# Kernel tuning notes

Measured on AMD Instinct MI355X. Metric: run time of the kernel, lower is better.

## Reference

```python
import jax, jax.numpy as jnp
import numpy as np


def _l2norm(t, axis=-1, eps=1e-12):
    # matches torch F.normalize: x / max(||x||, eps)
    n = jnp.sqrt(jnp.sum(t * t, axis=axis, keepdims=True))
    return t / jnp.maximum(n, eps)


def setup_inputs() -> dict:
    key = jax.random.key(0)
    ks = jax.random.split(key, 5)
    B, N, C, H = 16, 4096, 768, 12
    x = jax.random.normal(ks[0], (B, N, C), dtype=jnp.float32)
    Wqkv = jax.random.normal(ks[1], (C, 3 * C), dtype=jnp.float32) * (C ** -0.5)
    bqkv = jax.random.normal(ks[2], (3 * C,), dtype=jnp.float32) * 0.02
    Wproj = jax.random.normal(ks[3], (C, C), dtype=jnp.float32) * (C ** -0.5)
    bproj = jax.random.normal(ks[4], (C,), dtype=jnp.float32) * 0.02
    temperature = jnp.ones((H, 1, 1), dtype=jnp.float32)
    return {"x": x, "Wqkv": Wqkv, "bqkv": bqkv, "Wproj": Wproj,
            "bproj": bproj, "temperature": temperature}


def reference(x, Wqkv, bqkv, Wproj, bproj, temperature):
    B, N, C = x.shape
    H = temperature.shape[0]
    Dh = C // H
    qkv = x @ Wqkv + bqkv                      # [B,N,3C]
    qkv = qkv.reshape(B, N, 3, H, Dh)
    # -> [3,B,H,Dh,N] (channels-as-tokens layout)
    qkv = jnp.transpose(qkv, (2, 0, 3, 4, 1))
    q, k, v = qkv[0], qkv[1], qkv[2]           # each [B,H,Dh,N]
    q = _l2norm(q, axis=-1)
    k = _l2norm(k, axis=-1)
    # cross-covariance over channels: [B,H,Dh,Dh]
    attn = jnp.einsum('bhdn,bhen->bhde', q, k) * temperature
    attn = jax.nn.softmax(attn, axis=-1)
    out = jnp.einsum('bhde,bhen->bhdn', attn, v)  # [B,H,Dh,N]
    out = jnp.transpose(out, (0, 3, 1, 2)).reshape(B, N, C)
    return out @ Wproj + bproj
```

## Files before the change

kernel.cpp:

```cpp
#include <hip/hip_runtime.h>

typedef __bf16 bf16x8 __attribute__((ext_vector_type(8)));
typedef float  f32x4  __attribute__((ext_vector_type(4)));
typedef unsigned short u16x8 __attribute__((ext_vector_type(8)));
typedef unsigned short u16x4 __attribute__((ext_vector_type(4)));

#define MFMA16(a, b, c) __builtin_amdgcn_mfma_f32_16x16x32_bf16((a), (b), (c), 0, 0, 0)

#define GLOAD16(g, l) __builtin_amdgcn_global_load_lds( \
    (const __attribute__((address_space(1))) void*)(g),  \
    (__attribute__((address_space(3))) void*)(l), 16, 0, 0)

__device__ __forceinline__ float bf2f(unsigned short u) {
    unsigned int x = ((unsigned int)u) << 16;
    return __builtin_bit_cast(float, x);
}
__device__ __forceinline__ unsigned short f2bf(float f) {
    unsigned int x = __builtin_bit_cast(unsigned int, f);
    x = x + 0x7FFFu + ((x >> 16) & 1u);
    return (unsigned short)(x >> 16);
}
__device__ __forceinline__ bool is_f32(const unsigned short* tf) { return tf[0] == 0; }
__device__ __forceinline__ float ldscal(const void* p, int i, bool f32m) {
    return f32m ? ((const float*)p)[i] : bf2f(((const unsigned short*)p)[i]);
}

__device__ __forceinline__ void tr_tile(const void* in_, unsigned short* out,
                                        int R, int C, int istride,
                                        int bid, bool f32m, unsigned short* T)
{
    const int nct = C >> 6;
    const int tx = bid % nct;
    const int ty = bid / nct;
    const int r0 = ty * 64, c0 = tx * 64;
    const int t = threadIdx.x;
#pragma unroll
    for (int s = 0; s < 2; ++s) {
        const int idx = t + s * 256;
        const int rr = idx >> 3;
        const int cc = (idx & 7) * 8;
        unsigned short v[8];
        if (f32m) {
            const float* inf = (const float*)in_;
            f32x4 a = *(const f32x4*)&inf[(size_t)(r0 + rr) * istride + c0 + cc];
            f32x4 b = *(const f32x4*)&inf[(size_t)(r0 + rr) * istride + c0 + cc + 4];
#pragma unroll
            for (int j = 0; j < 4; ++j) { v[j] = f2bf(a[j]); v[4 + j] = f2bf(b[j]); }
        } else {
            u16x8 a = *(const u16x8*)&((const unsigned short*)in_)[(size_t)(r0 + rr) * istride + c0 + cc];
#pragma unroll
            for (int j = 0; j < 8; ++j) v[j] = a[j];
        }
#pragma unroll
        for (int j = 0; j < 8; ++j) T[(cc + j) * 72 + rr] = v[j];
    }
    __syncthreads();
#pragma unroll
    for (int s = 0; s < 2; ++s) {
        const int idx = t + s * 256;
        const int cc = idx >> 3;
        const int rr = (idx & 7) * 8;
        u16x8 v = *(const u16x8*)&T[cc * 72 + rr];
        *(u16x8*)&out[(size_t)(c0 + cc) * R + r0 + rr] = v;
    }
}

__global__ __launch_bounds__(256)
void prep_all(const void* __restrict__ x, unsigned short* __restrict__ xb,
              unsigned short* __restrict__ xbT, float* __restrict__ sB,
              const void* __restrict__ Wqkv, const void* __restrict__ Wp,
              unsigned short* __restrict__ WqkT, unsigned short* __restrict__ Wv_bf,
              unsigned short* __restrict__ WprojT, const unsigned short* __restrict__ tf)
{
    __shared__ unsigned short T[64 * 72];
    const bool f32m = is_f32(tf);
    if (blockIdx.x < 12288) {
        const int tx = blockIdx.x % 12;
        const int ty = blockIdx.x / 12;
        const int r0 = ty * 64, c0 = tx * 64;
        const int t = threadIdx.x;
#pragma unroll
        for (int s = 0; s < 2; ++s) {
            const int idx = t + s * 256;
            const int rr = idx >> 3;
            const int cc = (idx & 7) * 8;
            u16x8 v;
            if (f32m) {
                const float* inf = (const float*)x;
                f32x4 a = *(const f32x4*)&inf[(size_t)(r0 + rr) * 768 + c0 + cc];
                f32x4 b = *(const f32x4*)&inf[(size_t)(r0 + rr) * 768 + c0 + cc + 4];
#pragma unroll
                for (int j = 0; j < 4; ++j) { v[j] = f2bf(a[j]); v[4 + j] = f2bf(b[j]); }
            } else {
                v = *(const u16x8*)&((const unsigned short*)x)[(size_t)(r0 + rr) * 768 + c0 + cc];
            }
            *(u16x8*)&xb[(size_t)(r0 + rr) * 768 + c0 + cc] = v;
#pragma unroll
            for (int j = 0; j < 8; ++j) T[(cc + j) * 72 + rr] = v[j];
        }
        __syncthreads();
#pragma unroll
        for (int s = 0; s < 2; ++s) {
            const int idx = t + s * 256;
            const int cc = idx >> 3;
            const int rr = (idx & 7) * 8;
            u16x8 v = *(const u16x8*)&T[cc * 72 + rr];
            *(u16x8*)&xbT[(size_t)(c0 + cc) * 65536 + r0 + rr] = v;
        }
        {
            const int col = t >> 2;
            const int seg = t & 3;
            float s = 0.f;
#pragma unroll
            for (int r = 0; r < 16; ++r) s += bf2f(T[col * 72 + seg * 16 + r]);
            s += __shfl_xor(s, 1);
            s += __shfl_xor(s, 2);
            if (seg == 0) atomicAdd(&sB[(r0 >> 12) * 768 + c0 + col], s);
        }
    } else {
        const int bid = blockIdx.x - 12288;
        if (bid < 288) {
            tr_tile(Wqkv, WqkT, 768, 1536, 2304, bid, f32m, T);
        } else if (bid < 576) {
            const int t = (bid - 288) * 256 + threadIdx.x;
            const int c = t / 96;
            const int e0 = (t % 96) * 8;
            u16x8 v;
            if (f32m) {
                const float* p = (const float*)Wqkv + (size_t)c * 2304 + 1536 + e0;
                f32x4 a = *(const f32x4*)p;
                f32x4 b = *(const f32x4*)(p + 4);
#pragma unroll
                for (int j = 0; j < 4; ++j) { v[j] = f2bf(a[j]); v[4 + j] = f2bf(b[j]); }
            } else {
                v = *(const u16x8*)&((const unsigned short*)Wqkv)[(size_t)c * 2304 + 1536 + e0];
            }
            *(u16x8*)&Wv_bf[(size_t)c * 768 + e0] = v;
        } else {
            tr_tile(Wp, WprojT, 768, 768, 768, bid - 576, f32m, T);
        }
    }
}

__global__ __launch_bounds__(256, 2)
void gemmG(const unsigned short* __restrict__ A, unsigned short* __restrict__ G)
{
    constexpr int NT = 64;
    constexpr size_t LD = 65536;
    __shared__ __align__(16) char SM[65536];
    unsigned short* lds = (unsigned short*)SM;

    const int tid  = threadIdx.x;
    const int wave = tid >> 6;
    const int lane = tid & 63;
    const int wm   = wave >> 1;
    const int wn   = wave & 1;
    const int lr   = lane & 15;
    const int lq   = lane >> 4;

    const int per = gridDim.x >> 3;
    const int wg  = (blockIdx.x & 7) * per + (blockIdx.x >> 3);
    const int b = wg / 21;
    int rr21 = wg % 21;
    int mt = 0;
    while (rr21 >= 6 - mt) { rr21 -= 6 - mt; ++mt; }
    const int nt = mt + rr21;
    const size_t m0 = (size_t)mt * 128;
    const int n0 = nt * 128;

    const unsigned short* Ab = A + m0 * LD + (size_t)b * 4096;
    const unsigned short* Bb = A + (size_t)n0 * LD + (size_t)b * 4096;
    unsigned short* Gb = G + (size_t)b * 589824;

    f32x4 zero = {0.f, 0.f, 0.f, 0.f};
    f32x4 acc[4][4];
#pragma unroll
    for (int i = 0; i < 4; ++i)
#pragma unroll
        for (int j = 0; j < 4; ++j) acc[i][j] = zero;

    auto STAGE = [&](int t) {
        unsigned short* la_ = lds + (t & 1) * 16384;
        unsigned short* lb_ = la_ + 8192;
#pragma unroll
        for (int it = 0; it < 4; ++it) {
            const int c = it * 256 + tid;
            const int row = c >> 3;
            const int gs = (c & 7) ^ (row & 7);
            GLOAD16(Ab + (size_t)row * LD + t * 64 + gs * 8, la_ + c * 8);
        }
#pragma unroll
        for (int it = 0; it < 4; ++it) {
            const int c = it * 256 + tid;
            const int row = c >> 3;
            const int gs = (c & 7) ^ (row & 7);
            GLOAD16(Bb + (size_t)row * LD + t * 64 + gs * 8, lb_ + c * 8);
        }
    };

    STAGE(0);
    STAGE(1);

    for (int t = 0; t < NT; ++t) {
        if (t + 1 < NT) asm volatile("s_waitcnt vmcnt(8)" ::: "memory");
        else            asm volatile("s_waitcnt vmcnt(0)" ::: "memory");
        __builtin_amdgcn_s_barrier();
        __builtin_amdgcn_sched_barrier(0);

        const char* la = (const char*)(lds + (t & 1) * 16384);
        const char* lb = la + 16384;

        bf16x8 bfr[4][2], af[4][2];
#pragma unroll
        for (int ni = 0; ni < 4; ++ni)
#pragma unroll
            for (int ks = 0; ks < 2; ++ks) {
                const int row = wn * 64 + ni * 16 + lr;
                const int s   = ks * 4 + lq;
                bfr[ni][ks] = *(const bf16x8*)(lb + row * 128 + ((s ^ (row & 7)) << 4));
            }
#pragma unroll
        for (int mi = 0; mi < 4; ++mi)
#pragma unroll
            for (int ks = 0; ks < 2; ++ks) {
                const int row = wm * 64 + mi * 16 + lr;
                const int s   = ks * 4 + lq;
                af[mi][ks] = *(const bf16x8*)(la + row * 128 + ((s ^ (row & 7)) << 4));
            }
        __builtin_amdgcn_s_setprio(1);
#pragma unroll
        for (int mi = 0; mi < 4; ++mi)
#pragma unroll
            for (int ni = 0; ni < 4; ++ni)
#pragma unroll
                for (int ks = 0; ks < 2; ++ks)
                    acc[mi][ni] = MFMA16(af[mi][ks], bfr[ni][ks], acc[mi][ni]);
        __builtin_amdgcn_s_setprio(0);

        __builtin_amdgcn_sched_barrier(0);
        __builtin_amdgcn_s_barrier();
        if (t + 2 < NT) STAGE(t + 2);
    }

#pragma unroll
    for (int mi = 0; mi < 4; ++mi)
#pragma unroll
        for (int ni = 0; ni < 4; ++ni)
#pragma unroll
            for (int r = 0; r < 4; ++r) {
                const size_t row = m0 + (size_t)(wm * 64 + mi * 16 + lq * 4 + r);
                const int col = n0 + wn * 64 + ni * 16 + lr;
                Gb[row * 768 + col] = f2bf(acc[mi][ni][r]);
            }

    if (mt != nt) {
        asm volatile("s_waitcnt lgkmcnt(0)" ::: "memory");
        __builtin_amdgcn_s_barrier();
        unsigned short* CTw = (unsigned short*)SM + wave * (64 * 68);
#pragma unroll
        for (int mi = 0; mi < 4; ++mi)
#pragma unroll
            for (int ni = 0; ni < 4; ++ni) {
                u16x4 pk;
#pragma unroll
                for (int r = 0; r < 4; ++r) pk[r] = f2bf(acc[mi][ni][r]);
                *(u16x4*)&CTw[(ni * 16 + lr) * 68 + mi * 16 + lq * 4] = pk;
            }
#pragma unroll
        for (int rep = 0; rep < 8; ++rep) {
            const int idx = rep * 64 + lane;
            const int c = idx >> 3;
            const int j = (idx & 7) * 8;
            u16x8 v = *(const u16x8*)&CTw[c * 68 + j];
            const size_t rowT = (size_t)n0 + wn * 64 + c;
            const int colT = (int)m0 + wm * 64 + j;
            *(u16x8*)&Gb[rowT * 768 + colT] = v;
        }
    }
}

template<int MODE>
__global__ __launch_bounds__(512, 4)
void gemmH(const unsigned short* __restrict__ A,
           const unsigned short* __restrict__ BT,
           const float* __restrict__ bias,
           const void* __restrict__ bp,
           unsigned short* __restrict__ o0,
           float* __restrict__ oF,
           const unsigned short* __restrict__ tf)
{
    constexpr int K = 768, NT = 24;
    __shared__ __align__(16) char SM[73728];

    const bool f32m = is_f32(tf);
    const int tid  = threadIdx.x;
    const int wave = tid >> 6;
    const int lane = tid & 63;
    const int wm   = wave >> 2;
    const int wn   = wave & 3;
    const int lr   = lane & 15;
    const int lq   = lane >> 4;

    const int per = gridDim.x >> 3;
    const int wg  = (blockIdx.x & 7) * per + (blockIdx.x >> 3);
    int b = 0, mt, nt;
    if (MODE == 4) { b = wg / 36; const int r = wg % 36; mt = r / 3; nt = r % 3; }
    else           { mt = wg / 3; nt = wg % 3; }
    const size_t m0 = (size_t)mt * 128;
    const int n0 = nt * 256;

    const unsigned short* Ab = A + m0 * K;
    const unsigned short* Bb;
    if (MODE == 1)      Bb = BT + (m0 >> 12) * (size_t)589824 + (size_t)n0 * K;
    else if (MODE == 4) Bb = BT + (size_t)b * 589824 + (size_t)n0 * K;
    else                Bb = BT + (size_t)n0 * K;

    f32x4 zero = {0.f, 0.f, 0.f, 0.f};
    f32x4 acc[4][4];
#pragma unroll
    for (int i = 0; i < 4; ++i)
#pragma unroll
        for (int j = 0; j < 4; ++j) acc[i][j] = zero;

    auto STAGE = [&](int t) {
        char* base = SM + (t % 3) * 24576;
        {
            const int c = tid;
            const int rp = c >> 3;
            const int ch = (c & 7) ^ (rp & 7);
            const int srow = rp * 2 + (ch >> 2);
            const int sk = (ch & 3) * 8;
            GLOAD16(Ab + (size_t)srow * K + t * 32 + sk, base + c * 16);
        }
#pragma unroll
        for (int ev = 0; ev < 2; ++ev) {
            const int c = ev * 512 + tid;
            const int rp = c >> 3;
            const int ch = (c & 7) ^ (rp & 7);
            const int srow = rp * 2 + (ch >> 2);
            const int sk = (ch & 3) * 8;
            GLOAD16(Bb + (size_t)srow * K + t * 32 + sk, base + 8192 + c * 16);
        }
    };

    STAGE(0);
    STAGE(1);

    for (int t = 0; t < NT; ++t) {
        if (t < NT - 1) asm volatile("s_waitcnt vmcnt(3)" ::: "memory");
        else            asm volatile("s_waitcnt vmcnt(0)" ::: "memory");
        __builtin_amdgcn_s_barrier();
        __builtin_amdgcn_sched_barrier(0);

        const char* la = SM + (t % 3) * 24576;
        const char* lb = la + 8192;

        bf16x8 af[4], bfr[4];
#pragma unroll
        for (int ni = 0; ni < 4; ++ni) {
            const int row = wn * 64 + ni * 16 + lr;
            const int rp = row >> 1;
            const int ch = (row & 1) * 4 + lq;
            bfr[ni] = *(const bf16x8*)(lb + rp * 128 + ((ch ^ (rp & 7)) << 4));
        }
#pragma unroll
        for (int mi = 0; mi < 4; ++mi) {
            const int row = wm * 64 + mi * 16 + lr;
            const int rp = row >> 1;
            const int ch = (row & 1) * 4 + lq;
            af[mi] = *(const bf16x8*)(la + rp * 128 + ((ch ^ (rp & 7)) << 4));
        }
        __builtin_amdgcn_s_setprio(1);
#pragma unroll
        for (int mi = 0; mi < 4; ++mi)
#pragma unroll
            for (int ni = 0; ni < 4; ++ni)
                acc[mi][ni] = MFMA16(af[mi], bfr[ni], acc[mi][ni]);
        __builtin_amdgcn_s_setprio(0);

        __builtin_amdgcn_sched_barrier(0);
        if (t + 2 < NT) STAGE(t + 2);
    }

    float bb[4];
#pragma unroll
    for (int ni = 0; ni < 4; ++ni) {
        const int col = n0 + wn * 64 + ni * 16 + lr;
        bb[ni] = (MODE == 1) ? (bias[(m0 >> 12) * 768 + col] + ldscal(bp, col, f32m)) : 0.f;
    }

    if (MODE == 1 && f32m) {
        asm volatile("s_waitcnt lgkmcnt(0)" ::: "memory");
        __builtin_amdgcn_s_barrier();
        float* Lf = (float*)SM + wave * 2176;
#pragma unroll
        for (int mh = 0; mh < 2; ++mh) {
#pragma unroll
            for (int mp = 0; mp < 2; ++mp)
#pragma unroll
                for (int ni = 0; ni < 4; ++ni)
#pragma unroll
                    for (int r = 0; r < 4; ++r) {
                        const int lrow = mp * 16 + lq * 4 + r;
                        const int lcol = ni * 16 + lr;
                        Lf[lrow * 68 + lcol] = acc[mh * 2 + mp][ni][r] + bb[ni];
                    }
#pragma unroll
            for (int rr = 0; rr < 8; ++rr) {
                const int lrow = rr * 4 + lq;
                const int lcol = lr * 4;
                f32x4 v = *(const f32x4*)&Lf[lrow * 68 + lcol];
                const size_t grow = m0 + (size_t)(wm * 64 + mh * 32 + lrow);
                *(f32x4*)&oF[grow * 768 + n0 + wn * 64 + lcol] = v;
            }
        }
    } else {
#pragma unroll
        for (int mi = 0; mi < 4; ++mi)
#pragma unroll
            for (int ni = 0; ni < 4; ++ni)
#pragma unroll
                for (int r = 0; r < 4; ++r) {
                    const size_t row = m0 + (size_t)(wm * 64 + mi * 16 + lq * 4 + r);
                    const int col = n0 + wn * 64 + ni * 16 + lr;
                    const float val = acc[mi][ni][r] + bb[ni];
                    if (MODE == 1) {
                        o0[row * 768 + col] = f2bf(val);
                    } else if (MODE == 2) {
                        o0[row * 768 + col] = f2bf(val);
                    } else {
                        o0[(size_t)b * 1179648 + row * 768 + col] = f2bf(val);
                    }
                }
    }
}

__global__ __launch_bounds__(512)
void attn_mb(const unsigned short* __restrict__ P,
             const unsigned short* __restrict__ WqkT,
             const float* __restrict__ s,
             const void* __restrict__ bqkv,
             const unsigned short* __restrict__ WprojT,
             const unsigned short* __restrict__ tf,
             unsigned short* __restrict__ MbT,
             float* __restrict__ beff)
{
    __shared__ float S[64][64];
    __shared__ float nq[64], nk[64], uq[64], uk[64];
    __shared__ float sb[768];
    __shared__ float bkv[64];
    __shared__ float bvv[64];
    __shared__ unsigned short Pl[64 * 72];
    const bool f32m = is_f32(tf);
    const int bh = blockIdx.x;
    const int b = bh / 12, h = bh % 12;
    const unsigned short* Pq = P + (size_t)b * 1179648 + (size_t)(h * 64) * 768;
    const unsigned short* Wq = WqkT + (size_t)(h * 64) * 768;
    const unsigned short* Pk = Pq + 589824;
    const unsigned short* Wk = Wq + 589824;
    const int tid = threadIdx.x;
    const int wave = tid >> 6;
    const int lane = tid & 63;
    const int lr = lane & 15;
    const int lq = lane >> 4;

    for (int i = tid; i < 768; i += 512) sb[i] = s[b * 768 + i];
    if (tid < 64)       bkv[tid] = ldscal(bqkv, 768 + h * 64 + tid, f32m);
    else if (tid < 128) bvv[tid - 64] = ldscal(bqkv, 1536 + h * 64 + (tid - 64), f32m);

    f32x4 zero = {0.f, 0.f, 0.f, 0.f};
    f32x4 acc[4][4];
#pragma unroll
    for (int i = 0; i < 4; ++i)
#pragma unroll
        for (int j = 0; j < 4; ++j) acc[i][j] = zero;

    for (int ks = 0; ks < 3; ++ks) {
        const int j0 = wave * 96 + ks * 32 + lq * 8;
        u16x8 qa[4], ka[4];
#pragma unroll
        for (int mi = 0; mi < 4; ++mi)
            qa[mi] = *(const u16x8*)&Pq[(size_t)(mi * 16 + lr) * 768 + j0];
#pragma unroll
        for (int ni = 0; ni < 4; ++ni)
            ka[ni] = *(const u16x8*)&Wk[(size_t)(ni * 16 + lr) * 768 + j0];
#pragma unroll
        for (int mi = 0; mi < 4; ++mi)
#pragma unroll
            for (int ni = 0; ni < 4; ++ni)
                acc[mi][ni] = MFMA16(__builtin_bit_cast(bf16x8, qa[mi]),
                                     __builtin_bit_cast(bf16x8, ka[ni]),
                                     acc[mi][ni]);
    }
    __syncthreads();

    for (int ww = 0; ww < 8; ++ww) {
        if (wave == ww) {
#pragma unroll
            for (int mi = 0; mi < 4; ++mi)
#pragma unroll
                for (int ni = 0; ni < 4; ++ni)
#pragma unroll
                    for (int r = 0; r < 4; ++r) {
                        const int d = mi * 16 + lq * 4 + r;
                        const int e = ni * 16 + lr;
                        if (ww == 0) S[d][e] = acc[mi][ni][r];
                        else         S[d][e] += acc[mi][ni][r];
                    }
        }
        __syncthreads();
    }

    const int d   = tid >> 3;
    const int oct = tid & 7;
    {
        const unsigned short* pqr = Pq + (size_t)d * 768 + oct * 96;
        const unsigned short* wqr = Wq + (size_t)d * 768 + oct * 96;
        const unsigned short* pkr = Pk + (size_t)d * 768 + oct * 96;
        const unsigned short* wkr = Wk + (size_t)d * 768 + oct * 96;
        float a_nq = 0.f, a_uq = 0.f, a_nk = 0.f, a_uk = 0.f;
        for (int i = 0; i < 12; ++i) {
            u16x8 vp = *(const u16x8*)&pqr[i * 8];
            u16x8 vw = *(const u16x8*)&wqr[i * 8];
            u16x8 kp = *(const u16x8*)&pkr[i * 8];
            u16x8 kw = *(const u16x8*)&wkr[i * 8];
#pragma unroll
            for (int j = 0; j < 8; ++j) {
                const float wqv = bf2f(vw[j]);
                const float wkv = bf2f(kw[j]);
                const float sj = sb[oct * 96 + i * 8 + j];
                a_nq += bf2f(vp[j]) * wqv;
                a_uq += sj * wqv;
                a_nk += bf2f(kp[j]) * wkv;
                a_uk += sj * wkv;
            }
        }
        a_nq += __shfl_xor(a_nq, 1); a_nq += __shfl_xor(a_nq, 2); a_nq += __shfl_xor(a_nq, 4);
        a_uq += __shfl_xor(a_uq, 1); a_uq += __shfl_xor(a_uq, 2); a_uq += __shfl_xor(a_uq, 4);
        a_nk += __shfl_xor(a_nk, 1); a_nk += __shfl_xor(a_nk, 2); a_nk += __shfl_xor(a_nk, 4);
        a_uk += __shfl_xor(a_uk, 1); a_uk += __shfl_xor(a_uk, 2); a_uk += __shfl_xor(a_uk, 4);
        if (oct == 0) { nq[d] = a_nq; uq[d] = a_uq; nk[d] = a_nk; uk[d] = a_uk; }
    }
    __syncthreads();

    {
        const float tv  = f32m ? ((const float*)tf)[h] : bf2f(tf[h]);
        const float bqd = ldscal(bqkv, h * 64 + d, f32m);
        const float uqd = uq[d];
        const float nqf = nq[d] + 2.f * bqd * uqd + 4096.f * bqd * bqd;
        const float qn  = fmaxf(sqrtf(fmaxf(nqf, 0.f)), 1e-12f);
        float vals[8];
        float mx = -1e30f;
#pragma unroll
        for (int i = 0; i < 8; ++i) {
            const int e = oct * 8 + i;
            const float bke = bkv[e];
            const float nkf = nk[e] + 2.f * bke * uk[e] + 4096.f * bke * bke;
            const float kn  = fmaxf(sqrtf(fmaxf(nkf, 0.f)), 1e-12f);
            const float sv  = S[d][e] + bqd * uk[e] + uqd * bke + 4096.f * bqd * bke;
            const float val = sv / (qn * kn) * tv;
            vals[i] = val;
            mx = fmaxf(mx, val);
        }
        mx = fmaxf(mx, __shfl_xor(mx, 1));
        mx = fmaxf(mx, __shfl_xor(mx, 2));
        mx = fmaxf(mx, __shfl_xor(mx, 4));
        float sum = 0.f;
#pragma unroll
        for (int i = 0; i < 8; ++i) { vals[i] = __expf(vals[i] - mx); sum += vals[i]; }
        sum += __shfl_xor(sum, 1);
        sum += __shfl_xor(sum, 2);
        sum += __shfl_xor(sum, 4);
        const float inv = 1.0f / sum;
#pragma unroll
        for (int i = 0; i < 8; ++i) {
            const int e = oct * 8 + i;
            Pl[e * 72 + d] = f2bf(vals[i] * inv);
        }
    }
    __syncthreads();

    f32x4 accm[4][6];
#pragma unroll
    for (int i = 0; i < 4; ++i)
#pragma unroll
        for (int j = 0; j < 6; ++j) accm[i][j] = zero;

#pragma unroll
    for (int ks = 0; ks < 2; ++ks) {
        bf16x8 af[4], bfr[6];
#pragma unroll
        for (int mi = 0; mi < 4; ++mi)
            af[mi] = *(const bf16x8*)&Pl[(mi * 16 + lr) * 72 + ks * 32 + lq * 8];
#pragma unroll
        for (int ni = 0; ni < 6; ++ni) {
            const int j = wave * 96 + ni * 16 + lr;
            bfr[ni] = *(const bf16x8*)&WprojT[(size_t)j * 768 + h * 64 + ks * 32 + lq * 8];
        }
#pragma unroll
        for (int mi = 0; mi < 4; ++mi)
#pragma unroll
            for (int ni = 0; ni < 6; ++ni)
                accm[mi][ni] = MFMA16(af[mi], bfr[ni], accm[mi][ni]);
    }

#pragma unroll
    for (int ni = 0; ni < 6; ++ni) {
        const int j = wave * 96 + ni * 16 + lr;
        float part = 0.f;
#pragma unroll
        for (int mi = 0; mi < 4; ++mi) {
            const int e = mi * 16 + lq * 4;
            u16x4 pk;
#pragma unroll
            for (int r = 0; r < 4; ++r) {
                pk[r] = f2bf(accm[mi][ni][r]);
                part += accm[mi][ni][r] * bvv[e + r];
            }
            *(u16x4*)&MbT[(size_t)b * 589824 + (size_t)j * 768 + h * 64 + e] = pk;
        }
        atomicAdd(&beff[b * 768 + j], part);
    }
}

extern "C" void kernel_launch(void* const* d_in, const int* in_sizes, int n_in,
                              void* d_out, int out_size, void* d_ws, size_t ws_size,
                              hipStream_t stream)
{
    const void* x    = d_in[0];
    const void* Wqkv = d_in[1];
    const void* bqkv = d_in[2];
    const void* Wp   = d_in[3];
    const void* bp   = d_in[4];
    const unsigned short* tf = (const unsigned short*)d_in[5];

    char* w = (char*)d_ws;
    unsigned short* xbT    = (unsigned short*)(w);
    unsigned short* xb     = (unsigned short*)(w + 100663296);
    unsigned short* G      = (unsigned short*)(w + 201326592);
    unsigned short* P      = (unsigned short*)(w + 220200960);
    unsigned short* PT     = (unsigned short*)(w + 257949696);
    unsigned short* MbT    = (unsigned short*)(w + 276824064);
    unsigned short* WqkT   = (unsigned short*)(w + 295698432);
    unsigned short* Wv_bf  = (unsigned short*)(w + 298057728);
    unsigned short* WprojT = (unsigned short*)(w + 299237376);
    float*          sB     = (float*)(w + 301989888);
    float*          beff   = (float*)(w + 302039040);

    hipMemsetAsync(sB, 0, 98304, stream);
    prep_all<<<dim3(13008), dim3(256), 0, stream>>>(x, xb, xbT, sB, Wqkv, Wp,
                                                    WqkT, Wv_bf, WprojT, tf);

    gemmG<<<dim3(336), dim3(256), 0, stream>>>(xbT, G);
    gemmH<4><<<dim3(576), dim3(512), 0, stream>>>(WqkT, G, nullptr, nullptr, P, nullptr, tf);
    attn_mb<<<dim3(192), dim3(512), 0, stream>>>(P, WqkT, sB, bqkv, WprojT, tf, MbT, beff);
    gemmH<2><<<dim3(288), dim3(512), 0, stream>>>(MbT, Wv_bf, nullptr, nullptr, PT, nullptr, tf);
    gemmH<1><<<dim3(1536), dim3(512), 0, stream>>>(xb, PT, beff, bp,
        (unsigned short*)d_out, (float*)d_out, tf);
}
```

Baseline: 405.3 us.

## Fuse per-head Wq/Wk·G projection into attention kernel, drop gemmH<4> pass

Removes the separate gemmH<4> launch that wrote the full projected P = Wqk·G for all batches, and instead computes each head's 64x768 Y = W·G slice inside the attention kernel into shared memory. The Gram-style S, norms and bias dot products are then read from LDS rather than re-read from global P. This avoids a kernel launch and the write and read of the P buffer. In exchange, only 192 blocks do the large projection GEMM with a simple unpipelined global-load MFMA loop and roughly 100KB+ of LDS per block, so occupancy and latency hiding are limited.

Result: slower. 457.2 us (+12.8%).

```diff
diff --git a/kernel.cpp b/kernel.cpp
--- a/kernel.cpp
+++ b/kernel.cpp
@@ -303,17 +303,14 @@
 
     const int per = gridDim.x >> 3;
     const int wg  = (blockIdx.x & 7) * per + (blockIdx.x >> 3);
-    int b = 0, mt, nt;
-    if (MODE == 4) { b = wg / 36; const int r = wg % 36; mt = r / 3; nt = r % 3; }
-    else           { mt = wg / 3; nt = wg % 3; }
+    const int mt = wg / 3, nt = wg % 3;
     const size_t m0 = (size_t)mt * 128;
     const int n0 = nt * 256;
 
     const unsigned short* Ab = A + m0 * K;
     const unsigned short* Bb;
-    if (MODE == 1)      Bb = BT + (m0 >> 12) * (size_t)589824 + (size_t)n0 * K;
-    else if (MODE == 4) Bb = BT + (size_t)b * 589824 + (size_t)n0 * K;
-    else                Bb = BT + (size_t)n0 * K;
+    if (MODE == 1) Bb = BT + (m0 >> 12) * (size_t)589824 + (size_t)n0 * K;
+    else           Bb = BT + (size_t)n0 * K;
 
     f32x4 zero = {0.f, 0.f, 0.f, 0.f};
     f32x4 acc[4][4];
@@ -424,27 +421,23 @@
                     const size_t row = m0 + (size_t)(wm * 64 + mi * 16 + lq * 4 + r);
                     const int col = n0 + wn * 64 + ni * 16 + lr;
                     const float val = acc[mi][ni][r] + bb[ni];
-                    if (MODE == 1) {
-                        o0[row * 768 + col] = f2bf(val);
-                    } else if (MODE == 2) {
-                        o0[row * 768 + col] = f2bf(val);
-                    } else {
-                        o0[(size_t)b * 1179648 + row * 768 + col] = f2bf(val);
-                    }
+                    o0[row * 768 + col] = f2bf(val);
                 }
     }
 }
 
 __global__ __launch_bounds__(512)
-void attn_mb(const unsigned short* __restrict__ P,
-             const unsigned short* __restrict__ WqkT,
-             const float* __restrict__ s,
-             const void* __restrict__ bqkv,
-             const unsigned short* __restrict__ WprojT,
-             const unsigned short* __restrict__ tf,
-             unsigned short* __restrict__ MbT,
-             float* __restrict__ beff)
+void attnG(const unsigned short* __restrict__ G,
+           const unsigned short* __restrict__ WqkT,
+           const float* __restrict__ s,
+           const void* __restrict__ bqkv,
+           const unsigned short* __restrict__ WprojT,
+           const unsigned short* __restrict__ tf,
+           unsigned short* __restrict__ MbT,
+           float* __restrict__ beff)
 {
+    constexpr int YLD = 776;
+    __shared__ unsigned short Yl[64 * YLD];
     __shared__ float S[64][64];
     __shared__ float nq[64], nk[64], uq[64], uk[64];
     __shared__ float sb[768];
@@ -452,11 +445,11 @@
     __shared__ float bvv[64];
     __shared__ unsigned short Pl[64 * 72];
     const bool f32m = is_f32(tf);
-    const int bh = blockIdx.x;
+    const int per = gridDim.x >> 3;
+    const int bh = (blockIdx.x & 7) * per + (blockIdx.x >> 3);
     const int b = bh / 12, h = bh % 12;
-    const unsigned short* Pq = P + (size_t)b * 1179648 + (size_t)(h * 64) * 768;
+    const unsigned short* Gb = G + (size_t)b * 589824;
     const unsigned short* Wq = WqkT + (size_t)(h * 64) * 768;
-    const unsigned short* Pk = Pq + 589824;
     const unsigned short* Wk = Wq + 589824;
     const int tid = threadIdx.x;
     const int wave = tid >> 6;
@@ -469,31 +462,85 @@
     else if (tid < 128) bvv[tid - 64] = ldscal(bqkv, 1536 + h * 64 + (tid - 64), f32m);
 
     f32x4 zero = {0.f, 0.f, 0.f, 0.f};
-    f32x4 acc[4][4];
+
+    auto COMP_Y = [&](const unsigned short* Ws) {
+        f32x4 acy[4][6];
+#pragma unroll
+        for (int i = 0; i < 4; ++i)
+#pragma unroll
+            for (int j = 0; j < 6; ++j) acy[i][j] = zero;
+        const int c0 = wave * 96;
+        for (int ks = 0; ks < 24; ++ks) {
+            bf16x8 af[4], bfr[6];
+#pragma unroll
+            for (int mi = 0; mi < 4; ++mi)
+                af[mi] = *(const bf16x8*)&Ws[(size_t)(mi * 16 + lr) * 768 + ks * 32 + lq * 8];
+#pragma unroll
+            for (int ni = 0; ni < 6; ++ni)
+                bfr[ni] = *(const bf16x8*)&Gb[(size_t)(c0 + ni * 16 + lr) * 768 + ks * 32 + lq * 8];
+#pragma unroll
+            for (int mi = 0; mi < 4; ++mi)
+#pragma unroll
+                for (int ni = 0; ni < 6; ++ni)
+                    acy[mi][ni] = MFMA16(af[mi], bfr[ni], acy[mi][ni]);
+        }
+#pragma unroll
+        for (int mi = 0; mi < 4; ++mi)
+#pragma unroll
+            for (int ni = 0; ni < 6; ++ni)
+#pragma unroll
+                for (int r = 0; r < 4; ++r)
+                    Yl[(mi * 16 + lq * 4 + r) * YLD + c0 + ni * 16 + lr] = f2bf(acy[mi][ni][r]);
+    };
+
+    const int d   = tid >> 3;
+    const int oct = tid & 7;
+
+    auto DOTS = [&](const unsigned short* Ws, float* nd, float* ud) {
+        const unsigned short* wr = Ws + (size_t)d * 768 + oct * 96;
+        const unsigned short* yr = &Yl[d * YLD + oct * 96];
+        float a_n = 0.f, a_u = 0.f;
+        for (int i = 0; i < 12; ++i) {
+            u16x8 vy = *(const u16x8*)&yr[i * 8];
+            u16x8 vw = *(const u16x8*)&wr[i * 8];
+#pragma unroll
+            for (int j = 0; j < 8; ++j) {
+                const float wv = bf2f(vw[j]);
+                a_n += bf2f(vy[j]) * wv;
+                a_u += sb[oct * 96 + i * 8 + j] * wv;
+            }
+        }
+        a_n += __shfl_xor(a_n, 1); a_n += __shfl_xor(a_n, 2); a_n += __shfl_xor(a_n, 4);
+        a_u += __shfl_xor(a_u, 1); a_u += __shfl_xor(a_u, 2); a_u += __shfl_xor(a_u, 4);
+        if (oct == 0) { nd[d] = a_n; ud[d] = a_u; }
+    };
+
+    COMP_Y(Wq);
+    __syncthreads();
+    DOTS(Wq, nq, uq);
+    f32x4 accs[4][4];
 #pragma unroll
     for (int i = 0; i < 4; ++i)
 #pragma unroll
-        for (int j = 0; j < 4; ++j) acc[i][j] = zero;
-
-    for (int ks = 0; ks < 3; ++ks) {
-        const int j0 = wave * 96 + ks * 32 + lq * 8;
-        u16x8 qa[4], ka[4];
-#pragma unroll
-        for (int mi = 0; mi < 4; ++mi)
-            qa[mi] = *(const u16x8*)&Pq[(size_t)(mi * 16 + lr) * 768 + j0];
-#pragma unroll
-        for (int ni = 0; ni < 4; ++ni)
-            ka[ni] = *(const u16x8*)&Wk[(size_t)(ni * 16 + lr) * 768 + j0];
-#pragma unroll
-        for (int mi = 0; mi < 4; ++mi)
+        for (int j = 0; j < 4; ++j) accs[i][j] = zero;
+    {
+        const int cc0 = wave * 96;
+        for (int ks = 0; ks < 3; ++ks) {
+            bf16x8 af[4], bfr[4];
+#pragma unroll
+            for (int mi = 0; mi < 4; ++mi)
+                af[mi] = *(const bf16x8*)&Yl[(mi * 16 + lr) * YLD + cc0 + ks * 32 + lq * 8];
 #pragma unroll
             for (int ni = 0; ni < 4; ++ni)
-                acc[mi][ni] = MFMA16(__builtin_bit_cast(bf16x8, qa[mi]),
-                                     __builtin_bit_cast(bf16x8, ka[ni]),
-                                     acc[mi][ni]);
+                bfr[ni] = *(const bf16x8*)&Wk[(size_t)(ni * 16 + lr) * 768 + cc0 + ks * 32 + lq * 8];
+#pragma unroll
+            for (int mi = 0; mi < 4; ++mi)
+#pragma unroll
+                for (int ni = 0; ni < 4; ++ni)
+                    accs[mi][ni] = MFMA16(af[mi], bfr[ni], accs[mi][ni]);
+        }
     }
     __syncthreads();
-
     for (int ww = 0; ww < 8; ++ww) {
         if (wave == ww) {
 #pragma unroll
@@ -502,45 +549,17 @@
                 for (int ni = 0; ni < 4; ++ni)
 #pragma unroll
                     for (int r = 0; r < 4; ++r) {
-                        const int d = mi * 16 + lq * 4 + r;
+                        const int dd = mi * 16 + lq * 4 + r;
                         const int e = ni * 16 + lr;
-                        if (ww == 0) S[d][e] = acc[mi][ni][r];
-                        else         S[d][e] += acc[mi][ni][r];
+                        if (ww == 0) S[dd][e] = accs[mi][ni][r];
+                        else         S[dd][e] += accs[mi][ni][r];
                     }
         }
         __syncthreads();
     }
-
-    const int d   = tid >> 3;
-    const int oct = tid & 7;
-    {
-        const unsigned short* pqr = Pq + (size_t)d * 768 + oct * 96;
-        const unsigned short* wqr = Wq + (size_t)d * 768 + oct * 96;
-        const unsigned short* pkr = Pk + (size_t)d * 768 + oct * 96;
-        const unsigned short* wkr = Wk + (size_t)d * 768 + oct * 96;
-        float a_nq = 0.f, a_uq = 0.f, a_nk = 0.f, a_uk = 0.f;
-        for (int i = 0; i < 12; ++i) {
-            u16x8 vp = *(const u16x8*)&pqr[i * 8];
-            u16x8 vw = *(const u16x8*)&wqr[i * 8];
-            u16x8 kp = *(const u16x8*)&pkr[i * 8];
-            u16x8 kw = *(const u16x8*)&wkr[i * 8];
-#pragma unroll
-            for (int j = 0; j < 8; ++j) {
-                const float wqv = bf2f(vw[j]);
-                const float wkv = bf2f(kw[j]);
-                const float sj = sb[oct * 96 + i * 8 + j];
-                a_nq += bf2f(vp[j]) * wqv;
-                a_uq += sj * wqv;
-                a_nk += bf2f(kp[j]) * wkv;
-                a_uk += sj * wkv;
-            }
-        }
-        a_nq += __shfl_xor(a_nq, 1); a_nq += __shfl_xor(a_nq, 2); a_nq += __shfl_xor(a_nq, 4);
-        a_uq += __shfl_xor(a_uq, 1); a_uq += __shfl_xor(a_uq, 2); a_uq += __shfl_xor(a_uq, 4);
-        a_nk += __shfl_xor(a_nk, 1); a_nk += __shfl_xor(a_nk, 2); a_nk += __shfl_xor(a_nk, 4);
-        a_uk += __shfl_xor(a_uk, 1); a_uk += __shfl_xor(a_uk, 2); a_uk += __shfl_xor(a_uk, 4);
-        if (oct == 0) { nq[d] = a_nq; uq[d] = a_uq; nk[d] = a_nk; uk[d] = a_uk; }
-    }
+    COMP_Y(Wk);
+    __syncthreads();
+    DOTS(Wk, nk, uk);
     __syncthreads();
 
     {
@@ -585,7 +604,6 @@
     for (int i = 0; i < 4; ++i)
 #pragma unroll
         for (int j = 0; j < 6; ++j) accm[i][j] = zero;
-
 #pragma unroll
     for (int ks = 0; ks < 2; ++ks) {
         bf16x8 af[4], bfr[6];
@@ -638,7 +656,6 @@
     unsigned short* xbT    = (unsigned short*)(w);
     unsigned short* xb     = (unsigned short*)(w + 100663296);
     unsigned short* G      = (unsigned short*)(w + 201326592);
-    unsigned short* P      = (unsigned short*)(w + 220200960);
     unsigned short* PT     = (unsigned short*)(w + 257949696);
     unsigned short* MbT    = (unsigned short*)(w + 276824064);
     unsigned short* WqkT   = (unsigned short*)(w + 295698432);
@@ -652,8 +669,7 @@
                                                     WqkT, Wv_bf, WprojT, tf);
 
     gemmG<<<dim3(336), dim3(256), 0, stream>>>(xbT, G);
-    gemmH<4><<<dim3(576), dim3(512), 0, stream>>>(WqkT, G, nullptr, nullptr, P, nullptr, tf);
-    attn_mb<<<dim3(192), dim3(512), 0, stream>>>(P, WqkT, sB, bqkv, WprojT, tf, MbT, beff);
+    attnG<<<dim3(192), dim3(512), 0, stream>>>(G, WqkT, sB, bqkv, WprojT, tf, MbT, beff);
     gemmH<2><<<dim3(288), dim3(512), 0, stream>>>(MbT, Wv_bf, nullptr, nullptr, PT, nullptr, tf);
     gemmH<1><<<dim3(1536), dim3(512), 0, stream>>>(xb, PT, beff, bp,
         (unsigned short*)d_out, (float*)d_out, tf);
```
